# Kernel tuning notes

Hardware: AMD Instinct MI355X
Metric: run time of the kernel (lower is better)

Reference implementation:

```python
import jax, jax.numpy as jnp
import numpy as np


def feature_map(x):
    # phi(x) = elu(x) + 1 (ensures positivity)
    return jax.nn.elu(x) + 1.0


def setup_inputs() -> dict:
    key = jax.random.key(0)
    k0, k1, k2, k3 = jax.random.split(key, 4)
    B, T, d_model, D = 4, 4096, 1024, 128
    x = jax.random.normal(k0, (B, T, d_model), dtype=jnp.float32)
    s = 1.0 / np.sqrt(d_model)
    Wq = jax.random.normal(k1, (d_model, D), dtype=jnp.float32) * s
    Wk = jax.random.normal(k2, (d_model, D), dtype=jnp.float32) * s
    Wv = jax.random.normal(k3, (d_model, D), dtype=jnp.float32) * s
    return {"x": x, "Wq": Wq, "Wk": Wk, "Wv": Wv}


def _causal_linear_attention(phi_q, phi_k, v):
    # phi_q, phi_k: [B,T,D]; v: [B,T,Dv]
    B, T, D = phi_q.shape
    Dv = v.shape[-1]
    # time-major for scan: [T,B,D]
    qT = jnp.swapaxes(phi_q, 0, 1)
    kT = jnp.swapaxes(phi_k, 0, 1)
    vT = jnp.swapaxes(v, 0, 1)

    def step(carry, inp):
        kv, ks = carry                       # kv: [B,D,Dv], ks: [B,D]
        qt, kt, vt = inp                     # each [B,D] / [B,Dv]
        kv = kv + kt[:, :, None] * vt[:, None, :]   # k_t^T v_t outer product
        ks = ks + kt
        num = jnp.einsum('bd,bdv->bv', qt, kv)      # [B,Dv]
        den = jnp.einsum('bd,bd->b', qt, ks)[:, None]
        return (kv, ks), num / den

    init = (jnp.zeros((B, D, Dv), phi_q.dtype), jnp.zeros((B, D), phi_q.dtype))
    _, outT = jax.lax.scan(step, init, (qT, kT, vT))  # outT: [T,B,Dv]
    return jnp.swapaxes(outT, 0, 1)


def reference(x, Wq, Wk, Wv):
    q = x @ Wq
    k = x @ Wk
    v = x @ Wv
    phi_q = feature_map(q)
    phi_k = feature_map(k)
    # dropout is identity in eval mode
    return _causal_linear_attention(phi_q, phi_k, v)
```

## Files before the change

kernel.cpp:

```cpp
#include <hip/hip_runtime.h>

#define DMODEL 1024
#define DHEAD 128
#define CHUNK 128
#define NCHUNK 32

typedef __attribute__((ext_vector_type(4))) float f32x4;
typedef __attribute__((ext_vector_type(8))) short bf16x8;

__device__ __forceinline__ unsigned short f2bf(float f) {
  union { float f; unsigned u; } v; v.f = f;
  unsigned r = v.u + 0x7FFF + ((v.u >> 16) & 1);
  return (unsigned short)(r >> 16);
}
__device__ __forceinline__ float bf2f(unsigned short h) {
  union { unsigned u; float f; } v; v.u = ((unsigned)h) << 16;
  return v.f;
}
__device__ __forceinline__ unsigned cvtpk(float lo, float hi) {
  unsigned r;
  asm("v_cvt_pk_bf16_f32 %0, %1, %2" : "=v"(r) : "v"(lo), "v"(hi));
  return r;
}
__device__ __forceinline__ void gload16(const void* g, void* l) {
  __builtin_amdgcn_global_load_lds(
      (const __attribute__((address_space(1))) unsigned int*)g,
      (__attribute__((address_space(3))) unsigned int*)l, 16, 0, 0);
}

__global__ __launch_bounds__(256) void transpose_w_kernel(
    const float* __restrict__ Wq, const float* __restrict__ Wk,
    const float* __restrict__ Wv, unsigned short* __restrict__ WT) {
  int id = blockIdx.x * 256 + threadIdx.x;
  int w = id >> 17;
  int rem = id & 131071;
  int n = rem >> 10;
  int k = rem & 1023;
  const float* W = (w == 0) ? Wq : (w == 1) ? Wk : Wv;
  WT[id] = f2bf(W[(size_t)k * DHEAD + n]);
}

__global__ __launch_bounds__(128) void proj_kernel(
    const float* __restrict__ x, const unsigned short* __restrict__ WT,
    unsigned short* __restrict__ phiQ, unsigned short* __restrict__ phiK,
    unsigned short* __restrict__ Vb) {
  const int which = blockIdx.y;
  const unsigned short* Wt = WT + (size_t)which * (DHEAD * DMODEL);
  unsigned short* outp = (which == 0) ? phiQ : (which == 1) ? phiK : Vb;
  const int m0 = blockIdx.x * 64;

  __shared__ float xs[64][64];
  __shared__ unsigned short ws[128][64];

  const int tid = threadIdx.x;
  const int wave = tid >> 6;
  const int lane = tid & 63;
  const int lrow = lane & 15, kgrp = lane >> 4;

  f32x4 acc[2][8];
#pragma unroll
  for (int i = 0; i < 2; ++i)
#pragma unroll
    for (int j = 0; j < 8; ++j) acc[i][j] = (f32x4)0.0f;

  for (int kk = 0; kk < DMODEL; kk += 64) {
    if (kk) __syncthreads();
#pragma unroll
    for (int i = 0; i < 8; ++i) {
      int instr = i * 2 + wave;
      int row = instr * 4 + (lane >> 4);
      int slot = lane & 15;
      int gcol = (slot ^ (row & 7)) << 2;
      gload16(&x[(size_t)(m0 + row) * DMODEL + kk + gcol],
              (char*)xs + instr * 1024);
    }
#pragma unroll
    for (int i = 0; i < 8; ++i) {
      int instr = i * 2 + wave;
      int row = instr * 8 + (lane >> 3);
      int slot = lane & 7;
      int gcol = (slot ^ (row & 7)) << 3;
      gload16(&Wt[(size_t)row * DMODEL + kk + gcol],
              (char*)ws + instr * 1024);
    }
    __syncthreads();

#pragma unroll
    for (int ks2 = 0; ks2 < 2; ++ks2) {
      bf16x8 af[2];
#pragma unroll
      for (int mr = 0; mr < 2; ++mr) {
        int arow = wave * 32 + mr * 16 + lrow;
        int s0 = ks2 * 8 + kgrp * 2;
        const float4 f0 = *reinterpret_cast<const float4*>(
            &xs[arow][(s0 ^ (arow & 7)) << 2]);
        const float4 f1 = *reinterpret_cast<const float4*>(
            &xs[arow][((s0 + 1) ^ (arow & 7)) << 2]);
        union { unsigned u[4]; bf16x8 v; } p;
        p.u[0] = cvtpk(f0.x, f0.y);
        p.u[1] = cvtpk(f0.z, f0.w);
        p.u[2] = cvtpk(f1.x, f1.y);
        p.u[3] = cvtpk(f1.z, f1.w);
        af[mr] = p.v;
      }
#pragma unroll
      for (int nr = 0; nr < 8; ++nr) {
        int brow = nr * 16 + lrow;
        int bs = ks2 * 4 + kgrp;
        bf16x8 bf = *reinterpret_cast<const bf16x8*>(
            &ws[brow][(bs ^ (brow & 7)) << 3]);
        acc[0][nr] = __builtin_amdgcn_mfma_f32_16x16x32_bf16(af[0], bf, acc[0][nr], 0, 0, 0);
        acc[1][nr] = __builtin_amdgcn_mfma_f32_16x16x32_bf16(af[1], bf, acc[1][nr], 0, 0, 0);
      }
    }
  }
#pragma unroll
  for (int mr = 0; mr < 2; ++mr)
#pragma unroll
    for (int nr = 0; nr < 8; ++nr)
#pragma unroll
      for (int r = 0; r < 4; ++r) {
        int row = m0 + wave * 32 + mr * 16 + kgrp * 4 + r;
        int col = nr * 16 + lrow;
        float v = acc[mr][nr][r];
        if (which < 2) v = (v > 0.0f) ? (v + 1.0f) : __expf(v);
        outp[(size_t)row * DHEAD + col] = f2bf(v);
      }
}

__global__ __launch_bounds__(256) void chunkkv_kernel(
    const unsigned short* __restrict__ phiK, const unsigned short* __restrict__ Vb,
    float* __restrict__ KVc, float* __restrict__ ksc) {
  const size_t base = (size_t)blockIdx.x * CHUNK * DHEAD;
  __shared__ unsigned short kt[128][136];
  __shared__ unsigned short vt[128][136];
  __shared__ float csum[2][128];
  const int tid = threadIdx.x;
  const int wave = tid >> 6, lane = tid & 63;
  const int lrow = lane & 15, kgrp = lane >> 4;

#pragma unroll
  for (int it = 0; it < 8; ++it) {
    int idx = it * 256 + tid;
    int t = idx >> 4;
    int d0 = (idx & 15) << 3;
    uint4 k4 = *reinterpret_cast<const uint4*>(&phiK[base + (size_t)t * DHEAD + d0]);
    uint4 v4 = *reinterpret_cast<const uint4*>(&Vb[base + (size_t)t * DHEAD + d0]);
    const unsigned short* ks_ = reinterpret_cast<const unsigned short*>(&k4);
    const unsigned short* vs_ = reinterpret_cast<const unsigned short*>(&v4);
#pragma unroll
    for (int j = 0; j < 8; ++j) { kt[d0 + j][t] = ks_[j]; vt[d0 + j][t] = vs_[j]; }
  }
  __syncthreads();

  f32x4 acc[2][8];
#pragma unroll
  for (int i = 0; i < 2; ++i)
#pragma unroll
    for (int j = 0; j < 8; ++j) acc[i][j] = (f32x4)0.0f;
#pragma unroll
  for (int ks = 0; ks < 4; ++ks) {
    int t0 = ks * 32 + kgrp * 8;
    bf16x8 afrag[2];
#pragma unroll
    for (int tr = 0; tr < 2; ++tr)
      afrag[tr] = *reinterpret_cast<const bf16x8*>(&vt[wave * 32 + tr * 16 + lrow][t0]);
#pragma unroll
    for (int tc = 0; tc < 8; ++tc) {
      bf16x8 bfrag = *reinterpret_cast<const bf16x8*>(&kt[tc * 16 + lrow][t0]);
      acc[0][tc] = __builtin_amdgcn_mfma_f32_16x16x32_bf16(afrag[0], bfrag, acc[0][tc], 0, 0, 0);
      acc[1][tc] = __builtin_amdgcn_mfma_f32_16x16x32_bf16(afrag[1], bfrag, acc[1][tc], 0, 0, 0);
    }
  }
  float* KVout = KVc + (size_t)blockIdx.x * (DHEAD * DHEAD);
#pragma unroll
  for (int tr = 0; tr < 2; ++tr)
#pragma unroll
    for (int tc = 0; tc < 8; ++tc)
#pragma unroll
      for (int r = 0; r < 4; ++r) {
        int dv = wave * 32 + tr * 16 + kgrp * 4 + r;
        int d = tc * 16 + lrow;
        KVout[dv * DHEAD + d] = acc[tr][tc][r];
      }
  {
    int d = tid & 127, h = tid >> 7;
    float s = 0.0f;
    for (int t = h * 64; t < h * 64 + 64; ++t) s += bf2f(kt[d][t]);
    csum[h][d] = s;
  }
  __syncthreads();
  if (tid < 128) ksc[(size_t)blockIdx.x * DHEAD + tid] = csum[0][tid] + csum[1][tid];
}

__global__ __launch_bounds__(256) void prefix_kernel(
    const float* __restrict__ KVc, const float* __restrict__ ksc,
    unsigned short* __restrict__ KVp, float* __restrict__ ksp) {
  if (blockIdx.x < 256) {
    int id = blockIdx.x * 256 + threadIdx.x;
    int b = id >> 14;
    int e = id & 16383;
    size_t base = (size_t)b * NCHUNK * 16384 + e;
    float acc = 0.0f;
    for (int c = 0; c < NCHUNK; ++c) {
      KVp[base + (size_t)c * 16384] = f2bf(acc);
      acc += KVc[base + (size_t)c * 16384];
    }
  } else {
    for (int i = threadIdx.x; i < 512; i += 256) {
      int b = i >> 7, d = i & 127;
      size_t base = (size_t)b * NCHUNK * DHEAD + d;
      float acc = 0.0f;
      for (int c = 0; c < NCHUNK; ++c) {
        ksp[base + (size_t)c * DHEAD] = acc;
        acc += ksc[base + (size_t)c * DHEAD];
      }
    }
  }
}

__global__ __launch_bounds__(256) void out_kernel(
    const unsigned short* __restrict__ phiQ, const unsigned short* __restrict__ phiK,
    const unsigned short* __restrict__ Vb, const unsigned short* __restrict__ KVp,
    const float* __restrict__ ksp, float* __restrict__ outp) {
  const size_t base = (size_t)blockIdx.x * CHUNK * DHEAD;
  __shared__ unsigned short qb[128][136];
  __shared__ unsigned short kb[128][136];
  __shared__ unsigned short vb[128][136];
  __shared__ float dsum[2][128];
  __shared__ float ks_l[128];
  const int tid = threadIdx.x;
  const int wave = tid >> 6, lane = tid & 63;
  const int lrow = lane & 15, kgrp = lane >> 4;

#pragma unroll
  for (int it = 0; it < 8; ++it) {
    int idx = it * 256 + tid;
    int t = idx >> 4;
    int d0 = (idx & 15) << 3;
    uint4 q4 = *reinterpret_cast<const uint4*>(&phiQ[base + (size_t)t * DHEAD + d0]);
    uint4 k4 = *reinterpret_cast<const uint4*>(&phiK[base + (size_t)t * DHEAD + d0]);
    uint4 v4 = *reinterpret_cast<const uint4*>(&Vb[base + (size_t)t * DHEAD + d0]);
    *reinterpret_cast<uint4*>(&qb[t][d0]) = q4;
    *reinterpret_cast<uint4*>(&kb[t][d0]) = k4;
    const unsigned short* vs_ = reinterpret_cast<const unsigned short*>(&v4);
#pragma unroll
    for (int j = 0; j < 8; ++j) vb[d0 + j][t] = vs_[j];
  }
  if (tid < 128) ks_l[tid] = ksp[(size_t)blockIdx.x * DHEAD + tid];
  __syncthreads();

  f32x4 acc[2][8];
#pragma unroll
  for (int i = 0; i < 2; ++i)
#pragma unroll
    for (int j = 0; j < 8; ++j) acc[i][j] = (f32x4)0.0f;
#pragma unroll
  for (int ks = 0; ks < 4; ++ks) {
    int d0 = ks * 32 + kgrp * 8;
    bf16x8 afrag[2];
#pragma unroll
    for (int tr = 0; tr < 2; ++tr)
      afrag[tr] = *reinterpret_cast<const bf16x8*>(&qb[wave * 32 + tr * 16 + lrow][d0]);
#pragma unroll
    for (int tc = 0; tc < 8; ++tc) {
      bf16x8 bfrag = *reinterpret_cast<const bf16x8*>(&kb[tc * 16 + lrow][d0]);
      acc[0][tc] = __builtin_amdgcn_mfma_f32_16x16x32_bf16(afrag[0], bfrag, acc[0][tc], 0, 0, 0);
      acc[1][tc] = __builtin_amdgcn_mfma_f32_16x16x32_bf16(afrag[1], bfrag, acc[1][tc], 0, 0, 0);
    }
  }
  __syncthreads();
#pragma unroll
  for (int tr = 0; tr < 2; ++tr)
#pragma unroll
    for (int tc = 0; tc < 8; ++tc)
#pragma unroll
      for (int r = 0; r < 4; ++r) {
        int t = wave * 32 + tr * 16 + kgrp * 4 + r;
        int s = tc * 16 + lrow;
        float v = (s <= t) ? acc[tr][tc][r] : 0.0f;
        kb[t][s] = f2bf(v);
      }
  __syncthreads();
  {
    int d = tid & 127, h = tid >> 7;
    float s1 = 0.0f, s2 = 0.0f;
    for (int j = h * 64; j < h * 64 + 64; ++j) {
      s1 += bf2f(kb[d][j]);
      s2 += bf2f(qb[d][j]) * ks_l[j];
    }
    dsum[h][d] = s1 + s2;
  }
#pragma unroll
  for (int i = 0; i < 2; ++i)
#pragma unroll
    for (int j = 0; j < 8; ++j) acc[i][j] = (f32x4)0.0f;
#pragma unroll
  for (int ks = 0; ks < 4; ++ks) {
    int t0 = ks * 32 + kgrp * 8;
    bf16x8 afrag[2];
#pragma unroll
    for (int tr = 0; tr < 2; ++tr)
      afrag[tr] = *reinterpret_cast<const bf16x8*>(&kb[wave * 32 + tr * 16 + lrow][t0]);
#pragma unroll
    for (int tc = 0; tc < 8; ++tc) {
      bf16x8 bfrag = *reinterpret_cast<const bf16x8*>(&vb[tc * 16 + lrow][t0]);
      acc[0][tc] = __builtin_amdgcn_mfma_f32_16x16x32_bf16(afrag[0], bfrag, acc[0][tc], 0, 0, 0);
      acc[1][tc] = __builtin_amdgcn_mfma_f32_16x16x32_bf16(afrag[1], bfrag, acc[1][tc], 0, 0, 0);
    }
  }
  __syncthreads();
#pragma unroll
  for (int it = 0; it < 8; ++it) {
    int idx = it * 256 + tid;
    int dv = idx >> 4;
    int d0 = (idx & 15) << 3;
    uint4 c4 = *reinterpret_cast<const uint4*>(&KVp[(size_t)blockIdx.x * 16384 + (size_t)dv * DHEAD + d0]);
    *reinterpret_cast<uint4*>(&vb[dv][d0]) = c4;
  }
  __syncthreads();
#pragma unroll
  for (int ks = 0; ks < 4; ++ks) {
    int d0 = ks * 32 + kgrp * 8;
    bf16x8 afrag[2];
#pragma unroll
    for (int tr = 0; tr < 2; ++tr)
      afrag[tr] = *reinterpret_cast<const bf16x8*>(&qb[wave * 32 + tr * 16 + lrow][d0]);
#pragma unroll
    for (int tc = 0; tc < 8; ++tc) {
      bf16x8 bfrag = *reinterpret_cast<const bf16x8*>(&vb[tc * 16 + lrow][d0]);
      acc[0][tc] = __builtin_amdgcn_mfma_f32_16x16x32_bf16(afrag[0], bfrag, acc[0][tc], 0, 0, 0);
      acc[1][tc] = __builtin_amdgcn_mfma_f32_16x16x32_bf16(afrag[1], bfrag, acc[1][tc], 0, 0, 0);
    }
  }
#pragma unroll
  for (int tr = 0; tr < 2; ++tr)
#pragma unroll
    for (int tc = 0; tc < 8; ++tc)
#pragma unroll
      for (int r = 0; r < 4; ++r) {
        int t = wave * 32 + tr * 16 + kgrp * 4 + r;
        int dv = tc * 16 + lrow;
        outp[base + (size_t)t * DHEAD + dv] = acc[tr][tc][r] / (dsum[0][t] + dsum[1][t]);
      }
}

extern "C" void kernel_launch(void* const* d_in, const int* in_sizes, int n_in,
                              void* d_out, int out_size, void* d_ws, size_t ws_size,
                              hipStream_t stream) {
  const float* x  = (const float*)d_in[0];
  const float* Wq = (const float*)d_in[1];
  const float* Wk = (const float*)d_in[2];
  const float* Wv = (const float*)d_in[3];
  float* out = (float*)d_out;
  char* ws = (char*)d_ws;
  unsigned short* phiQ = (unsigned short*)(ws + 0);
  unsigned short* phiK = (unsigned short*)(ws + 4194304);
  unsigned short* Vb   = (unsigned short*)(ws + 8388608);
  unsigned short* WT   = (unsigned short*)(ws + 12582912);
  float*          KVc  = (float*)(ws + 13369344);
  unsigned short* KVp  = (unsigned short*)(ws + 21757952);
  float*          ksc  = (float*)(ws + 25952256);
  float*          ksp  = (float*)(ws + 26017792);

  transpose_w_kernel<<<1536, 256, 0, stream>>>(Wq, Wk, Wv, WT);
  proj_kernel<<<dim3(256, 3), 128, 0, stream>>>(x, WT, phiQ, phiK, Vb);
  chunkkv_kernel<<<128, 256, 0, stream>>>(phiK, Vb, KVc, ksc);
  prefix_kernel<<<257, 256, 0, stream>>>(KVc, ksc, KVp, ksp);
  out_kernel<<<128, 256, 0, stream>>>(phiQ, phiK, Vb, KVp, ksp, out);
}
```

Baseline: 65.19 us.

## Double-buffer projection tiles and split output kernel across two query halves

The projection kernel now double-buffers its x and weight LDS tiles, prefetching the next K slice with async global-to-LDS loads while MFMAs run on the current one, using explicit vmcnt waits and barriers. The output kernel is split so each block handles 64 query rows of a chunk (grid 128x2), and the first half skips the fully masked upper key block. This doubles the number of blocks on a kernel that previously launched only 128. The chunk-KV transpose load pattern is also reordered to change LDS write bank conflicts. The cost is duplicated K/V/KVp loads across the two blocks per chunk and more LDS per projection block.

```diff
diff --git a/kernel.cpp b/kernel.cpp
--- a/kernel.cpp
+++ b/kernel.cpp
@@ -40,6 +40,30 @@
   WT[id] = f2bf(W[(size_t)k * DHEAD + n]);
 }
 
+__device__ __forceinline__ void stage_tiles(
+    const float* __restrict__ x, const unsigned short* __restrict__ Wt,
+    int m0, int kk, float (*xsb)[64], unsigned short (*wsb)[64],
+    int wave, int lane) {
+#pragma unroll
+  for (int i = 0; i < 8; ++i) {
+    int instr = i * 2 + wave;
+    int row = instr * 4 + (lane >> 4);
+    int slot = lane & 15;
+    int gcol = (slot ^ (row & 7)) << 2;
+    gload16(&x[(size_t)(m0 + row) * DMODEL + kk + gcol],
+            (char*)xsb + instr * 1024);
+  }
+#pragma unroll
+  for (int i = 0; i < 8; ++i) {
+    int instr = i * 2 + wave;
+    int row = instr * 8 + (lane >> 3);
+    int slot = lane & 7;
+    int gcol = (slot ^ (row & 7)) << 3;
+    gload16(&Wt[(size_t)row * DMODEL + kk + gcol],
+            (char*)wsb + instr * 1024);
+  }
+}
+
 __global__ __launch_bounds__(128) void proj_kernel(
     const float* __restrict__ x, const unsigned short* __restrict__ WT,
     unsigned short* __restrict__ phiQ, unsigned short* __restrict__ phiK,
@@ -49,8 +73,8 @@
   unsigned short* outp = (which == 0) ? phiQ : (which == 1) ? phiK : Vb;
   const int m0 = blockIdx.x * 64;
 
-  __shared__ float xs[64][64];
-  __shared__ unsigned short ws[128][64];
+  __shared__ float xs[2][64][64];
+  __shared__ unsigned short wsl[2][128][64];
 
   const int tid = threadIdx.x;
   const int wave = tid >> 6;
@@ -63,27 +87,17 @@
 #pragma unroll
     for (int j = 0; j < 8; ++j) acc[i][j] = (f32x4)0.0f;
 
+  stage_tiles(x, Wt, m0, 0, xs[0], wsl[0], wave, lane);
+  int cur = 0;
   for (int kk = 0; kk < DMODEL; kk += 64) {
-    if (kk) __syncthreads();
-#pragma unroll
-    for (int i = 0; i < 8; ++i) {
-      int instr = i * 2 + wave;
-      int row = instr * 4 + (lane >> 4);
-      int slot = lane & 15;
-      int gcol = (slot ^ (row & 7)) << 2;
-      gload16(&x[(size_t)(m0 + row) * DMODEL + kk + gcol],
-              (char*)xs + instr * 1024);
-    }
-#pragma unroll
-    for (int i = 0; i < 8; ++i) {
-      int instr = i * 2 + wave;
-      int row = instr * 8 + (lane >> 3);
-      int slot = lane & 7;
-      int gcol = (slot ^ (row & 7)) << 3;
-      gload16(&Wt[(size_t)row * DMODEL + kk + gcol],
-              (char*)ws + instr * 1024);
-    }
-    __syncthreads();
+    if (kk + 64 < DMODEL) {
+      stage_tiles(x, Wt, m0, kk + 64, xs[cur ^ 1], wsl[cur ^ 1], wave, lane);
+      asm volatile("s_waitcnt vmcnt(16)" ::: "memory");
+    } else {
+      asm volatile("s_waitcnt vmcnt(0)" ::: "memory");
+    }
+    __builtin_amdgcn_s_barrier();
+    __builtin_amdgcn_sched_barrier(0);
 
 #pragma unroll
     for (int ks2 = 0; ks2 < 2; ++ks2) {
@@ -93,9 +107,9 @@
         int arow = wave * 32 + mr * 16 + lrow;
         int s0 = ks2 * 8 + kgrp * 2;
         const float4 f0 = *reinterpret_cast<const float4*>(
-            &xs[arow][(s0 ^ (arow & 7)) << 2]);
+            &xs[cur][arow][(s0 ^ (arow & 7)) << 2]);
         const float4 f1 = *reinterpret_cast<const float4*>(
-            &xs[arow][((s0 + 1) ^ (arow & 7)) << 2]);
+            &xs[cur][arow][((s0 + 1) ^ (arow & 7)) << 2]);
         union { unsigned u[4]; bf16x8 v; } p;
         p.u[0] = cvtpk(f0.x, f0.y);
         p.u[1] = cvtpk(f0.z, f0.w);
@@ -108,11 +122,14 @@
         int brow = nr * 16 + lrow;
         int bs = ks2 * 4 + kgrp;
         bf16x8 bf = *reinterpret_cast<const bf16x8*>(
-            &ws[brow][(bs ^ (brow & 7)) << 3]);
+            &wsl[cur][brow][(bs ^ (brow & 7)) << 3]);
         acc[0][nr] = __builtin_amdgcn_mfma_f32_16x16x32_bf16(af[0], bf, acc[0][nr], 0, 0, 0);
         acc[1][nr] = __builtin_amdgcn_mfma_f32_16x16x32_bf16(af[1], bf, acc[1][nr], 0, 0, 0);
       }
     }
+    __builtin_amdgcn_sched_barrier(0);
+    __builtin_amdgcn_s_barrier();
+    cur ^= 1;
   }
 #pragma unroll
   for (int mr = 0; mr < 2; ++mr)
@@ -139,17 +156,18 @@
   const int wave = tid >> 6, lane = tid & 63;
   const int lrow = lane & 15, kgrp = lane >> 4;
 
-#pragma unroll
-  for (int it = 0; it < 8; ++it) {
-    int idx = it * 256 + tid;
-    int t = idx >> 4;
-    int d0 = (idx & 15) << 3;
-    uint4 k4 = *reinterpret_cast<const uint4*>(&phiK[base + (size_t)t * DHEAD + d0]);
-    uint4 v4 = *reinterpret_cast<const uint4*>(&Vb[base + (size_t)t * DHEAD + d0]);
-    const unsigned short* ks_ = reinterpret_cast<const unsigned short*>(&k4);
-    const unsigned short* vs_ = reinterpret_cast<const unsigned short*>(&v4);
-#pragma unroll
-    for (int j = 0; j < 8; ++j) { kt[d0 + j][t] = ks_[j]; vt[d0 + j][t] = vs_[j]; }
+  {
+    int t = tid & 127, dp = tid >> 7;
+#pragma unroll
+    for (int i = 0; i < 8; ++i) {
+      int d0 = (dp + 2 * i) * 8;
+      uint4 k4 = *reinterpret_cast<const uint4*>(&phiK[base + (size_t)t * DHEAD + d0]);
+      uint4 v4 = *reinterpret_cast<const uint4*>(&Vb[base + (size_t)t * DHEAD + d0]);
+      const unsigned short* kp = reinterpret_cast<const unsigned short*>(&k4);
+      const unsigned short* vp = reinterpret_cast<const unsigned short*>(&v4);
+#pragma unroll
+      for (int j = 0; j < 8; ++j) { kt[d0 + j][t] = kp[j]; vt[d0 + j][t] = vp[j]; }
+    }
   }
   __syncthreads();
 
@@ -184,10 +202,10 @@
         KVout[dv * DHEAD + d] = acc[tr][tc][r];
       }
   {
-    int d = tid & 127, h = tid >> 7;
+    int d = tid & 127, hh = tid >> 7;
     float s = 0.0f;
-    for (int t = h * 64; t < h * 64 + 64; ++t) s += bf2f(kt[d][t]);
-    csum[h][d] = s;
+    for (int t = hh * 64; t < hh * 64 + 64; ++t) s += bf2f(kt[d][t]);
+    csum[hh][d] = s;
   }
   __syncthreads();
   if (tid < 128) ksc[(size_t)blockIdx.x * DHEAD + tid] = csum[0][tid] + csum[1][tid];
@@ -223,126 +241,188 @@
     const unsigned short* __restrict__ phiQ, const unsigned short* __restrict__ phiK,
     const unsigned short* __restrict__ Vb, const unsigned short* __restrict__ KVp,
     const float* __restrict__ ksp, float* __restrict__ outp) {
-  const size_t base = (size_t)blockIdx.x * CHUNK * DHEAD;
-  __shared__ unsigned short qb[128][136];
+  const int c = blockIdx.x;
+  const int h = blockIdx.y;
+  const size_t kvbase = (size_t)c * CHUNK * DHEAD;
+  const size_t qbase = kvbase + (size_t)h * 64 * DHEAD;
+  __shared__ unsigned short qb[64][136];
   __shared__ unsigned short kb[128][136];
-  __shared__ unsigned short vb[128][136];
-  __shared__ float dsum[2][128];
+  __shared__ unsigned short vt[128][136];
+  __shared__ float dsum[4][64];
   __shared__ float ks_l[128];
   const int tid = threadIdx.x;
   const int wave = tid >> 6, lane = tid & 63;
   const int lrow = lane & 15, kgrp = lane >> 4;
 
 #pragma unroll
-  for (int it = 0; it < 8; ++it) {
+  for (int it = 0; it < 4; ++it) {
     int idx = it * 256 + tid;
     int t = idx >> 4;
     int d0 = (idx & 15) << 3;
-    uint4 q4 = *reinterpret_cast<const uint4*>(&phiQ[base + (size_t)t * DHEAD + d0]);
-    uint4 k4 = *reinterpret_cast<const uint4*>(&phiK[base + (size_t)t * DHEAD + d0]);
-    uint4 v4 = *reinterpret_cast<const uint4*>(&Vb[base + (size_t)t * DHEAD + d0]);
-    *reinterpret_cast<uint4*>(&qb[t][d0]) = q4;
-    *reinterpret_cast<uint4*>(&kb[t][d0]) = k4;
-    const unsigned short* vs_ = reinterpret_cast<const unsigned short*>(&v4);
-#pragma unroll
-    for (int j = 0; j < 8; ++j) vb[d0 + j][t] = vs_[j];
-  }
-  if (tid < 128) ks_l[tid] = ksp[(size_t)blockIdx.x * DHEAD + tid];
-  __syncthreads();
-
-  f32x4 acc[2][8];
-#pragma unroll
-  for (int i = 0; i < 2; ++i)
-#pragma unroll
-    for (int j = 0; j < 8; ++j) acc[i][j] = (f32x4)0.0f;
-#pragma unroll
-  for (int ks = 0; ks < 4; ++ks) {
-    int d0 = ks * 32 + kgrp * 8;
-    bf16x8 afrag[2];
-#pragma unroll
-    for (int tr = 0; tr < 2; ++tr)
-      afrag[tr] = *reinterpret_cast<const bf16x8*>(&qb[wave * 32 + tr * 16 + lrow][d0]);
-#pragma unroll
-    for (int tc = 0; tc < 8; ++tc) {
-      bf16x8 bfrag = *reinterpret_cast<const bf16x8*>(&kb[tc * 16 + lrow][d0]);
-      acc[0][tc] = __builtin_amdgcn_mfma_f32_16x16x32_bf16(afrag[0], bfrag, acc[0][tc], 0, 0, 0);
-      acc[1][tc] = __builtin_amdgcn_mfma_f32_16x16x32_bf16(afrag[1], bfrag, acc[1][tc], 0, 0, 0);
-    }
-  }
-  __syncthreads();
-#pragma unroll
-  for (int tr = 0; tr < 2; ++tr)
+    *reinterpret_cast<uint4*>(&qb[t][d0]) =
+        *reinterpret_cast<const uint4*>(&phiQ[qbase + (size_t)t * DHEAD + d0]);
+  }
+  if (tid < 128) ks_l[tid] = ksp[(size_t)c * DHEAD + tid];
+  if (h == 0) {
+#pragma unroll
+    for (int it = 0; it < 4; ++it) {
+      int idx = it * 256 + tid;
+      int t = idx >> 4;
+      int d0 = (idx & 15) << 3;
+      *reinterpret_cast<uint4*>(&kb[t][d0]) =
+          *reinterpret_cast<const uint4*>(&phiK[kvbase + (size_t)t * DHEAD + d0]);
+    }
+    int t = tid & 63, dp = tid >> 6;
+#pragma unroll
+    for (int i = 0; i < 4; ++i) {
+      int d0 = (dp + 4 * i) * 8;
+      uint4 v4 = *reinterpret_cast<const uint4*>(&Vb[kvbase + (size_t)t * DHEAD + d0]);
+      const unsigned short* vp = reinterpret_cast<const unsigned short*>(&v4);
+#pragma unroll
+      for (int j = 0; j < 8; ++j) vt[d0 + j][t] = vp[j];
+    }
+  } else {
+#pragma unroll
+    for (int it = 0; it < 8; ++it) {
+      int idx = it * 256 + tid;
+      int t = idx >> 4;
+      int d0 = (idx & 15) << 3;
+      *reinterpret_cast<uint4*>(&kb[t][d0]) =
+          *reinterpret_cast<const uint4*>(&phiK[kvbase + (size_t)t * DHEAD + d0]);
+    }
+    int t = tid & 127, dp = tid >> 7;
+#pragma unroll
+    for (int i = 0; i < 8; ++i) {
+      int d0 = (dp + 2 * i) * 8;
+      uint4 v4 = *reinterpret_cast<const uint4*>(&Vb[kvbase + (size_t)t * DHEAD + d0]);
+      const unsigned short* vp = reinterpret_cast<const unsigned short*>(&v4);
+#pragma unroll
+      for (int j = 0; j < 8; ++j) vt[d0 + j][t] = vp[j];
+    }
+  }
+  __syncthreads();
+
+  if (h == 0) {
+    f32x4 sa[4];
+#pragma unroll
+    for (int i = 0; i < 4; ++i) sa[i] = (f32x4)0.0f;
+#pragma unroll
+    for (int ks = 0; ks < 4; ++ks) {
+      int d0 = ks * 32 + kgrp * 8;
+      bf16x8 af = *reinterpret_cast<const bf16x8*>(&qb[wave * 16 + lrow][d0]);
+#pragma unroll
+      for (int tc = 0; tc < 4; ++tc) {
+        bf16x8 bf = *reinterpret_cast<const bf16x8*>(&kb[tc * 16 + lrow][d0]);
+        sa[tc] = __builtin_amdgcn_mfma_f32_16x16x32_bf16(af, bf, sa[tc], 0, 0, 0);
+      }
+    }
+    __syncthreads();
+#pragma unroll
+    for (int tc = 0; tc < 4; ++tc)
+#pragma unroll
+      for (int r = 0; r < 4; ++r) {
+        int trow = wave * 16 + kgrp * 4 + r;
+        int s = tc * 16 + lrow;
+        kb[trow][s] = f2bf((s <= trow) ? sa[tc][r] : 0.0f);
+      }
+  } else {
+    f32x4 sa[8];
+#pragma unroll
+    for (int i = 0; i < 8; ++i) sa[i] = (f32x4)0.0f;
+#pragma unroll
+    for (int ks = 0; ks < 4; ++ks) {
+      int d0 = ks * 32 + kgrp * 8;
+      bf16x8 af = *reinterpret_cast<const bf16x8*>(&qb[wave * 16 + lrow][d0]);
+#pragma unroll
+      for (int tc = 0; tc < 8; ++tc) {
+        bf16x8 bf = *reinterpret_cast<const bf16x8*>(&kb[tc * 16 + lrow][d0]);
+        sa[tc] = __builtin_amdgcn_mfma_f32_16x16x32_bf16(af, bf, sa[tc], 0, 0, 0);
+      }
+    }
+    __syncthreads();
 #pragma unroll
     for (int tc = 0; tc < 8; ++tc)
 #pragma unroll
       for (int r = 0; r < 4; ++r) {
-        int t = wave * 32 + tr * 16 + kgrp * 4 + r;
+        int trow = wave * 16 + kgrp * 4 + r;
         int s = tc * 16 + lrow;
-        float v = (s <= t) ? acc[tr][tc][r] : 0.0f;
-        kb[t][s] = f2bf(v);
-      }
-  __syncthreads();
+        kb[trow][s] = f2bf((s <= 64 + trow) ? sa[tc][r] : 0.0f);
+      }
+  }
+  __syncthreads();
+
   {
-    int d = tid & 127, h = tid >> 7;
-    float s1 = 0.0f, s2 = 0.0f;
-    for (int j = h * 64; j < h * 64 + 64; ++j) {
-      s1 += bf2f(kb[d][j]);
-      s2 += bf2f(qb[d][j]) * ks_l[j];
-    }
-    dsum[h][d] = s1 + s2;
-  }
-#pragma unroll
-  for (int i = 0; i < 2; ++i)
-#pragma unroll
-    for (int j = 0; j < 8; ++j) acc[i][j] = (f32x4)0.0f;
-#pragma unroll
-  for (int ks = 0; ks < 4; ++ks) {
-    int t0 = ks * 32 + kgrp * 8;
-    bf16x8 afrag[2];
-#pragma unroll
-    for (int tr = 0; tr < 2; ++tr)
-      afrag[tr] = *reinterpret_cast<const bf16x8*>(&kb[wave * 32 + tr * 16 + lrow][t0]);
-#pragma unroll
-    for (int tc = 0; tc < 8; ++tc) {
-      bf16x8 bfrag = *reinterpret_cast<const bf16x8*>(&vb[tc * 16 + lrow][t0]);
-      acc[0][tc] = __builtin_amdgcn_mfma_f32_16x16x32_bf16(afrag[0], bfrag, acc[0][tc], 0, 0, 0);
-      acc[1][tc] = __builtin_amdgcn_mfma_f32_16x16x32_bf16(afrag[1], bfrag, acc[1][tc], 0, 0, 0);
-    }
-  }
-  __syncthreads();
+    int t = tid & 63, h4 = tid >> 6;
+    float s = 0.0f;
+    if (h4 < 2) {
+      if (h4 * 64 < (h + 1) * 64) {
+        for (int j = h4 * 64; j < h4 * 64 + 64; ++j) s += bf2f(kb[t][j]);
+      }
+    } else {
+      for (int j = (h4 - 2) * 64; j < (h4 - 2) * 64 + 64; ++j)
+        s += bf2f(qb[t][j]) * ks_l[j];
+    }
+    dsum[h4][t] = s;
+  }
+
+  f32x4 acc[8];
+#pragma unroll
+  for (int i = 0; i < 8; ++i) acc[i] = (f32x4)0.0f;
+  if (h == 0) {
+#pragma unroll
+    for (int ks = 0; ks < 2; ++ks) {
+      int t0 = ks * 32 + kgrp * 8;
+      bf16x8 af = *reinterpret_cast<const bf16x8*>(&kb[wave * 16 + lrow][t0]);
+#pragma unroll
+      for (int tc = 0; tc < 8; ++tc) {
+        bf16x8 bf = *reinterpret_cast<const bf16x8*>(&vt[tc * 16 + lrow][t0]);
+        acc[tc] = __builtin_amdgcn_mfma_f32_16x16x32_bf16(af, bf, acc[tc], 0, 0, 0);
+      }
+    }
+  } else {
+#pragma unroll
+    for (int ks = 0; ks < 4; ++ks) {
+      int t0 = ks * 32 + kgrp * 8;
+      bf16x8 af = *reinterpret_cast<const bf16x8*>(&kb[wave * 16 + lrow][t0]);
+#pragma unroll
+      for (int tc = 0; tc < 8; ++tc) {
+        bf16x8 bf = *reinterpret_cast<const bf16x8*>(&vt[tc * 16 + lrow][t0]);
+        acc[tc] = __builtin_amdgcn_mfma_f32_16x16x32_bf16(af, bf, acc[tc], 0, 0, 0);
+      }
+    }
+  }
+  __syncthreads();
+
 #pragma unroll
   for (int it = 0; it < 8; ++it) {
     int idx = it * 256 + tid;
     int dv = idx >> 4;
     int d0 = (idx & 15) << 3;
-    uint4 c4 = *reinterpret_cast<const uint4*>(&KVp[(size_t)blockIdx.x * 16384 + (size_t)dv * DHEAD + d0]);
-    *reinterpret_cast<uint4*>(&vb[dv][d0]) = c4;
-  }
-  __syncthreads();
+    *reinterpret_cast<uint4*>(&vt[dv][d0]) =
+        *reinterpret_cast<const uint4*>(&KVp[(size_t)c * 16384 + (size_t)dv * DHEAD + d0]);
+  }
+  __syncthreads();
+
 #pragma unroll
   for (int ks = 0; ks < 4; ++ks) {
     int d0 = ks * 32 + kgrp * 8;
-    bf16x8 afrag[2];
-#pragma unroll
-    for (int tr = 0; tr < 2; ++tr)
-      afrag[tr] = *reinterpret_cast<const bf16x8*>(&qb[wave * 32 + tr * 16 + lrow][d0]);
+    bf16x8 af = *reinterpret_cast<const bf16x8*>(&qb[wave * 16 + lrow][d0]);
 #pragma unroll
     for (int tc = 0; tc < 8; ++tc) {
-      bf16x8 bfrag = *reinterpret_cast<const bf16x8*>(&vb[tc * 16 + lrow][d0]);
-      acc[0][tc] = __builtin_amdgcn_mfma_f32_16x16x32_bf16(afrag[0], bfrag, acc[0][tc], 0, 0, 0);
-      acc[1][tc] = __builtin_amdgcn_mfma_f32_16x16x32_bf16(afrag[1], bfrag, acc[1][tc], 0, 0, 0);
-    }
-  }
-#pragma unroll
-  for (int tr = 0; tr < 2; ++tr)
-#pragma unroll
-    for (int tc = 0; tc < 8; ++tc)
-#pragma unroll
-      for (int r = 0; r < 4; ++r) {
-        int t = wave * 32 + tr * 16 + kgrp * 4 + r;
-        int dv = tc * 16 + lrow;
-        outp[base + (size_t)t * DHEAD + dv] = acc[tr][tc][r] / (dsum[0][t] + dsum[1][t]);
-      }
+      bf16x8 bf = *reinterpret_cast<const bf16x8*>(&vt[tc * 16 + lrow][d0]);
+      acc[tc] = __builtin_amdgcn_mfma_f32_16x16x32_bf16(af, bf, acc[tc], 0, 0, 0);
+    }
+  }
+
+#pragma unroll
+  for (int tc = 0; tc < 8; ++tc)
+#pragma unroll
+    for (int r = 0; r < 4; ++r) {
+      int trow = wave * 16 + kgrp * 4 + r;
+      int dv = tc * 16 + lrow;
+      float den = dsum[0][trow] + dsum[1][trow] + dsum[2][trow] + dsum[3][trow];
+      outp[qbase + (size_t)trow * DHEAD + dv] = acc[tc][r] / den;
+    }
 }
 
 extern "C" void kernel_launch(void* const* d_in, const int* in_sizes, int n_in,
@@ -367,5 +447,5 @@
   proj_kernel<<<dim3(256, 3), 128, 0, stream>>>(x, WT, phiQ, phiK, Vb);
   chunkkv_kernel<<<128, 256, 0, stream>>>(phiK, Vb, KVc, ksc);
   prefix_kernel<<<257, 256, 0, stream>>>(KVc, ksc, KVp, ksp);
-  out_kernel<<<128, 256, 0, stream>>>(phiQ, phiK, Vb, KVp, ksp, out);
-}
+  out_kernel<<<dim3(128, 2), 256, 0, stream>>>(phiQ, phiK, Vb, KVp, ksp, out);
+}
```

Measured after the change: 77.18 us. 1.18x slower.
